# Optimization experiments

Measured on AMD Instinct MI355X. Metric: run time of the kernel, lower is better.

## Reference

```python
import jax, jax.numpy as jnp
import numpy as np

B, IN, C, M = 256, 512, 4, 6
S1, S2 = 255, 63          # neurons per layer excluding the prepended bias unit
K = 2 ** M                # contexts per neuron
P = 1e-3                  # pred_clipping
LMIN = float(np.log(P / (1.0 - P)))
LMAX = -LMIN
LR = 1e-3                 # constant learning rate
WCLIP = 5.0               # weight_clipping
BASE_BIAS = 0.0           # fixed base bias logit (original draws uniform in [LMIN, LMAX])


def setup_inputs() -> dict:
    key = jax.random.key(0)
    ks = jax.random.split(key, 10)
    x = jax.random.uniform(ks[0], (B, IN), dtype=jnp.float32)
    target = jax.random.randint(ks[1], (B,), 0, C, dtype=jnp.int32)
    cmaps1 = jax.random.normal(ks[2], (C, S1, M, IN), dtype=jnp.float32)
    w1 = jax.random.uniform(ks[3], (C, S1, K, IN), dtype=jnp.float32) * (2.0 / IN)
    bias1 = jax.random.uniform(ks[4], (1, 1, C), dtype=jnp.float32, minval=LMIN, maxval=LMAX)
    cmaps2 = jax.random.normal(ks[5], (C, S2, M, IN), dtype=jnp.float32)
    w2 = jax.random.uniform(ks[6], (C, S2, K, S1 + 1), dtype=jnp.float32) * (2.0 / (S1 + 1))
    bias2 = jax.random.uniform(ks[7], (1, 1, C), dtype=jnp.float32, minval=LMIN, maxval=LMAX)
    cmaps3 = jax.random.normal(ks[8], (C, 1, M, IN), dtype=jnp.float32)
    w3 = jax.random.uniform(ks[9], (C, 1, K, S2 + 1), dtype=jnp.float32) * (2.0 / (S2 + 1))
    return {"x": x, "target": target, "cmaps1": cmaps1, "w1": w1, "bias1": bias1,
            "cmaps2": cmaps2, "w2": w2, "bias2": bias2, "cmaps3": cmaps3, "w3": w3}


def _layer(logit3, context, tgt, cmaps, weights, bias):
    # logit3: (B, I, Cin) with Cin in {1, C}; context: (B, IN); tgt: (B, C) one-hot
    # cmaps: (C, S, M, IN); weights: (C, S, K, I)
    Cn, S = weights.shape[0], weights.shape[1]
    Bn = context.shape[0]
    # context halfspace gating -> per-(class, neuron, sample) context index
    dist = jnp.einsum('csmk,bk->csmb', cmaps, context)          # (C,S,M,B)
    conv = (2 ** jnp.arange(M, dtype=jnp.int32)).reshape(1, 1, M, 1)
    idx = jnp.sum((dist > 0.0).astype(jnp.int32) * conv, axis=2)  # (C,S,B)
    ci = jnp.arange(Cn)[:, None, None]
    si = jnp.arange(S)[None, :, None]
    sel = weights[ci, si, idx]                                  # gather: (C,S,B,I)
    lg = jnp.broadcast_to(logit3, (Bn, logit3.shape[1], Cn))    # (B,I,C)
    out = jnp.clip(jnp.einsum('csbi,bic->csb', sel, lg), LMIN, LMAX)
    out_t = jnp.transpose(out, (2, 1, 0))                       # (B,S,C)
    # online gradient-style update scattered back into the weight table
    diff = jax.nn.sigmoid(out_t) - tgt[:, None, :]              # (B,S,C)
    upd = LR * diff[..., None] * jnp.transpose(lg, (0, 2, 1))[:, None, :, :]  # (B,S,C,I)
    new_w = weights.at[ci, si, idx].set(
        jnp.clip(sel - jnp.transpose(upd, (2, 1, 0, 3)), -WCLIP, WCLIP))
    if bias is not None:
        out_t = jnp.concatenate([jnp.broadcast_to(bias, (Bn, 1, Cn)), out_t], axis=1)
    return out_t, new_w


def reference(x, target, cmaps1, w1, bias1, cmaps2, w2, bias2, cmaps3, w3):
    tgt = jax.nn.one_hot(target, C, dtype=x.dtype)              # (B,C)
    xb = jnp.clip(x, P, 1.0 - P)
    l0 = jnp.log(xb / (1.0 - xb)).at[:, 0].set(BASE_BIAS)       # base predictions in logit space
    out1, nw1 = _layer(l0[:, :, None], x, tgt, cmaps1, w1, bias1)  # (B,256,C)
    out2, nw2 = _layer(out1, x, tgt, cmaps2, w2, bias2)            # (B,64,C)
    out3, nw3 = _layer(out2, x, tgt, cmaps3, w3, None)             # (B,1,C)
    logits = out3[:, 0, :]                                         # (B,C)
    return (logits, nw1, nw2, nw3)
```

## Files before the change

### kernel.cpp

```cpp
#include <hip/hip_runtime.h>
#include <math.h>

#define B_   256
#define IN_  512
#define C_   4
#define M_   6
#define K_   64
#define S1_  255
#define S2_  63

#define NBLK1 (C_ * S1_)
#define NBLK2 (C_ * S2_)
#define NBLK3 (C_)
#define NBLK_ALL (NBLK1 + NBLK2 + NBLK3)

#define LMIN_ (-6.906754778648554f)
#define LMAX_ ( 6.906754778648554f)
#define LR_   0.001f
#define WCLIP_ 5.0f

typedef float v4f __attribute__((ext_vector_type(4)));

__device__ __forceinline__ float clampf(float v, float lo, float hi) {
    return fminf(fmaxf(v, lo), hi);
}

__global__ __launch_bounds__(256) void prep_kernel(const float* __restrict__ x,
                                                   const float* __restrict__ bias1,
                                                   const float* __restrict__ bias2,
                                                   float* __restrict__ xT,
                                                   float* __restrict__ l0,
                                                   float* __restrict__ l0T,
                                                   float* __restrict__ out1T,
                                                   float* __restrict__ out1RM,
                                                   float* __restrict__ out2T,
                                                   float* __restrict__ out2RM) {
    __shared__ float tx_[32][33];
    __shared__ float tl_[32][33];
    const int i0 = (blockIdx.x & 15) * 32;
    const int b0 = (blockIdx.x >> 4) * 32;
    const int tx = threadIdx.x & 31;
    const int ty = threadIdx.x >> 5;
#pragma unroll
    for (int r = 0; r < 4; ++r) {
        int bb = b0 + ty + 8 * r;
        int ii = i0 + tx;
        float xv = x[(size_t)bb * IN_ + ii];
        float xc = clampf(xv, 0.001f, 0.999f);
        float lv = (ii == 0) ? 0.0f : logf(xc / (1.0f - xc));
        l0[(size_t)bb * IN_ + ii] = lv;
        tx_[ty + 8 * r][tx] = xv;
        tl_[ty + 8 * r][tx] = lv;
    }
    __syncthreads();
#pragma unroll
    for (int r = 0; r < 4; ++r) {
        int ii = i0 + ty + 8 * r;
        int bb = b0 + tx;
        xT[(size_t)ii * B_ + bb]  = tx_[tx][ty + 8 * r];
        l0T[(size_t)ii * B_ + bb] = tl_[tx][ty + 8 * r];
    }
    int gid = blockIdx.x * 256 + threadIdx.x;
    if (gid < C_ * B_) {
        int c = gid >> 8, b = gid & 255;
        float b1 = bias1[c], b2 = bias2[c];
        out1T[((size_t)c * (S1_ + 1)) * B_ + b] = b1;
        out1RM[((size_t)c * B_ + b) * (S1_ + 1)] = b1;
        out2T[((size_t)c * (S2_ + 1)) * B_ + b] = b2;
        out2RM[((size_t)c * B_ + b) * (S2_ + 1)] = b2;
    }
}

__global__ __launch_bounds__(256) void route_kernel(
    const float* __restrict__ xT,
    const float* __restrict__ cmaps1,
    const float* __restrict__ cmaps2,
    const float* __restrict__ cmaps3,
    int* __restrict__ idx_buf)
{
    __shared__ float sacc[3][2][M_][B_];
    const int wv   = __builtin_amdgcn_readfirstlane(threadIdx.x >> 6);
    const int lane = threadIdx.x & 63;
    const int t0   = blockIdx.x * 2;

    const float* cmp[2];
#pragma unroll
    for (int u = 0; u < 2; ++u) {
        int bid = t0 + u;
        if (bid < NBLK1)              cmp[u] = cmaps1 + (size_t)bid * M_ * IN_;
        else if (bid < NBLK1 + NBLK2) cmp[u] = cmaps2 + (size_t)(bid - NBLK1) * M_ * IN_;
        else                          cmp[u] = cmaps3 + (size_t)(bid - NBLK1 - NBLK2) * M_ * IN_;
    }

    float acc[2][4][M_];
#pragma unroll
    for (int u = 0; u < 2; ++u)
#pragma unroll
        for (int jb = 0; jb < 4; ++jb)
#pragma unroll
            for (int m = 0; m < M_; ++m) acc[u][jb][m] = 0.0f;

    const int kw = wv * 128;
    for (int k0 = kw; k0 < kw + 128; k0 += 8) {
        float xv[8][4];
#pragma unroll
        for (int j = 0; j < 8; ++j)
#pragma unroll
            for (int jb = 0; jb < 4; ++jb)
                xv[j][jb] = xT[(size_t)(k0 + j) * B_ + 64 * jb + lane];
#pragma unroll
        for (int j = 0; j < 8; ++j)
#pragma unroll
            for (int u = 0; u < 2; ++u)
#pragma unroll
                for (int m = 0; m < M_; ++m) {
                    float cv = cmp[u][(size_t)m * IN_ + k0 + j];
#pragma unroll
                    for (int jb = 0; jb < 4; ++jb)
                        acc[u][jb][m] = fmaf(cv, xv[j][jb], acc[u][jb][m]);
                }
    }

    if (wv > 0) {
#pragma unroll
        for (int u = 0; u < 2; ++u)
#pragma unroll
            for (int jb = 0; jb < 4; ++jb)
#pragma unroll
                for (int m = 0; m < M_; ++m)
                    sacc[wv - 1][u][m][64 * jb + lane] = acc[u][jb][m];
    }
    __syncthreads();
    if (wv == 0) {
#pragma unroll
        for (int u = 0; u < 2; ++u)
#pragma unroll
            for (int jb = 0; jb < 4; ++jb) {
                int b = 64 * jb + lane;
                int myidx = 0;
#pragma unroll
                for (int m = 0; m < M_; ++m) {
                    float t = acc[u][jb][m] + sacc[0][u][m][b] + sacc[1][u][m][b] + sacc[2][u][m][b];
                    myidx |= (t > 0.0f) ? (1 << m) : 0;
                }
                idx_buf[(size_t)(t0 + u) * B_ + b] = myidx;
            }
    }
}

template<int DIN>
__device__ __forceinline__ void dotfin_body(
    int tile,
    const float* __restrict__ lgT, long lgT_sc,
    const float* __restrict__ w,
    const int* __restrict__ idx_buf,
    const int* __restrict__ target,
    float* __restrict__ onextT,
    float* __restrict__ onextRM,
    int* __restrict__ win_g,
    float* __restrict__ dw_g,
    int S,
    float* wl, float* part_s, float* diff_s, int* win_s)
{
    constexpr int HALF = DIN / 2;
    constexpr int NR   = HALF / 64;
    const int c   = tile / S;
    const int s   = tile - c * S;
    const int tid = threadIdx.x;
    const int kh  = __builtin_amdgcn_readfirstlane(tid >> 8);
    const int b   = tid & 255;

    if (tid < K_) win_s[tid] = -1;
    const int myrow = idx_buf[(size_t)tile * B_ + b];

    const float* wp  = w + (size_t)tile * K_ * DIN + kh * HALF;
    float*       dst = wl + kh * (K_ * 65);
    float dot = 0.0f;
#pragma unroll
    for (int r = 0; r < NR; ++r) {
        const float* src = wp + r * 64;
#pragma unroll
        for (int j = 0; j < 4; ++j) {
            int f   = b + 256 * j;
            int row = f >> 4;
            int q   = (f & 15) << 2;
            float4 v = *(const float4*)(src + (size_t)row * DIN + q);
            dst[row * 65 + q + 0] = v.x;
            dst[row * 65 + q + 1] = v.y;
            dst[row * 65 + q + 2] = v.z;
            dst[row * 65 + q + 3] = v.w;
        }
        __syncthreads();
        const float* lgp = lgT + (size_t)c * lgT_sc + (size_t)(kh * HALF + r * 64) * B_ + b;
        const float* wr  = dst + myrow * 65;
        for (int kk = 0; kk < 64; kk += 8) {
            float lv[8];
#pragma unroll
            for (int t = 0; t < 8; ++t) lv[t] = lgp[(size_t)(kk + t) * B_];
#pragma unroll
            for (int t = 0; t < 8; ++t) dot = fmaf(wr[kk + t], lv[t], dot);
        }
        __syncthreads();
    }
    if (kh == 1) part_s[b] = dot;
    __syncthreads();
    if (kh == 0) {
        float total = dot + part_s[b];
        float outv = clampf(total, LMIN_, LMAX_);
        onextT[((size_t)c * (S + 1) + (s + 1)) * B_ + b] = outv;
        onextRM[((size_t)c * B_ + b) * (size_t)(S + 1) + (s + 1)] = outv;
        float tg = (target[b] == c) ? 1.0f : 0.0f;
        diff_s[b] = 1.0f / (1.0f + expf(-outv)) - tg;
        atomicMax(&win_s[myrow], b);
    }
    __syncthreads();
    if (tid < K_) {
        int bw = win_s[tid];
        win_g[(size_t)tile * K_ + tid] = bw;
        dw_g[(size_t)tile * K_ + tid]  = (bw >= 0) ? LR_ * diff_s[bw] : 0.0f;
    }
}

template<int DIN>
__device__ __forceinline__ void update_body(
    int ub,
    const float* __restrict__ w,
    const float* __restrict__ lgRM, long lg_sc,
    const int* __restrict__ win_g,
    const float* __restrict__ dw_g,
    float* __restrict__ nw,
    int SK)
{
    constexpr int QPR = DIN / 4;
    constexpr int QSH = (DIN == 512) ? 7 : 6;
    const int base = ub * 2048 + threadIdx.x;
#pragma unroll
    for (int j = 0; j < 4; ++j) {
        int Q   = base + j * 512;
        int row = Q >> QSH;
        int col = (Q & (QPR - 1)) << 2;
        float4 wv = *(const float4*)(w + (size_t)row * DIN + col);
        int bw = win_g[row];
        if (bw >= 0) {
            float d = dw_g[row];
            int cc  = row / SK;
            const float4 lv = *(const float4*)(lgRM + (size_t)cc * lg_sc + (size_t)bw * DIN + col);
            wv.x = clampf(wv.x - d * lv.x, -WCLIP_, WCLIP_);
            wv.y = clampf(wv.y - d * lv.y, -WCLIP_, WCLIP_);
            wv.z = clampf(wv.z - d * lv.z, -WCLIP_, WCLIP_);
            wv.w = clampf(wv.w - d * lv.w, -WCLIP_, WCLIP_);
        }
        v4f o = {wv.x, wv.y, wv.z, wv.w};
        __builtin_nontemporal_store(o, (v4f*)(nw + (size_t)row * DIN + col));
    }
}

__global__ __launch_bounds__(512) void dotfin1_kernel(
    const float* __restrict__ l0T,
    const float* __restrict__ w1,
    const int* __restrict__ idx1,
    const int* __restrict__ target,
    float* __restrict__ out1T, float* __restrict__ out1RM,
    int* __restrict__ win1, float* __restrict__ dw1)
{
    __shared__ float wl[2 * K_ * 65];
    __shared__ float part_s[B_];
    __shared__ float diff_s[B_];
    __shared__ int   win_s[K_];
    dotfin_body<512>(blockIdx.x, l0T, 0L, w1, idx1, target,
                     out1T, out1RM, win1, dw1, S1_, wl, part_s, diff_s, win_s);
}

__global__ __launch_bounds__(512) void mix2_kernel(
    const float* __restrict__ out1T,
    const float* __restrict__ w2,
    const int* __restrict__ idx2,
    const int* __restrict__ target,
    float* __restrict__ out2T, float* __restrict__ out2RM,
    int* __restrict__ win2, float* __restrict__ dw2,
    const float* __restrict__ w1,
    const float* __restrict__ l0,
    const int* __restrict__ win1, const float* __restrict__ dw1,
    float* __restrict__ nw1, int ndot)
{
    __shared__ float wl[2 * K_ * 65];
    __shared__ float part_s[B_];
    __shared__ float diff_s[B_];
    __shared__ int   win_s[K_];
    if ((int)blockIdx.x < ndot)
        dotfin_body<256>(blockIdx.x, out1T, (long)(S1_ + 1) * B_, w2, idx2, target,
                         out2T, out2RM, win2, dw2, S2_, wl, part_s, diff_s, win_s);
    else
        update_body<512>(blockIdx.x - ndot, w1, l0, 0L, win1, dw1, nw1, S1_ * K_);
}

__device__ __forceinline__ void dotfinup3_body(
    int c,
    const float* __restrict__ lgT, long lgT_sc,
    const float* __restrict__ lgRM, long lg_sc,
    const float* __restrict__ w3,
    const int* __restrict__ idx3,
    const int* __restrict__ target,
    float* __restrict__ nw3,
    float* __restrict__ logits,
    float* wl , float* part_s, float* diff_s, float* dw_s, int* win_s)
{
    const int tid = threadIdx.x;
    const int kh  = __builtin_amdgcn_readfirstlane(tid >> 8);
    const int b   = tid & 255;
    if (tid < K_) win_s[tid] = -1;
    const int myrow = idx3[(size_t)c * B_ + b];

    const float* wp  = w3 + (size_t)c * K_ * 64 + kh * 32;
    float*       dst = wl + kh * (K_ * 33);
#pragma unroll
    for (int j = 0; j < 2; ++j) {
        int f   = b + 256 * j;
        int row = f >> 3;
        int q   = (f & 7) << 2;
        float4 v = *(const float4*)(wp + (size_t)row * 64 + q);
        dst[row * 33 + q + 0] = v.x;
        dst[row * 33 + q + 1] = v.y;
        dst[row * 33 + q + 2] = v.z;
        dst[row * 33 + q + 3] = v.w;
    }
    __syncthreads();
    const float* lgp = lgT + (size_t)c * lgT_sc + (size_t)(kh * 32) * B_ + b;
    const float* wr  = dst + myrow * 33;
    float dot = 0.0f;
    for (int kk = 0; kk < 32; kk += 8) {
        float lv[8];
#pragma unroll
        for (int t = 0; t < 8; ++t) lv[t] = lgp[(size_t)(kk + t) * B_];
#pragma unroll
        for (int t = 0; t < 8; ++t) dot = fmaf(wr[kk + t], lv[t], dot);
    }
    if (kh == 1) part_s[b] = dot;
    __syncthreads();
    if (kh == 0) {
        float total = dot + part_s[b];
        float outv = clampf(total, LMIN_, LMAX_);
        logits[(size_t)b * C_ + c] = outv;
        float tg = (target[b] == c) ? 1.0f : 0.0f;
        diff_s[b] = 1.0f / (1.0f + expf(-outv)) - tg;
        atomicMax(&win_s[myrow], b);
    }
    __syncthreads();
    if (tid < K_) dw_s[tid] = (win_s[tid] >= 0) ? LR_ * diff_s[win_s[tid]] : 0.0f;
    __syncthreads();

    const float* lgc = lgRM + (size_t)c * lg_sc;
    float* nwp = nw3 + (size_t)c * K_ * 64;
#pragma unroll
    for (int j = 0; j < 2; ++j) {
        int Q   = tid + 512 * j;
        int row = Q >> 4;
        int col = (Q & 15) << 2;
        const float* wsrc = wl + (col >> 5) * (K_ * 33) + row * 33 + (col & 31);
        float4 wv = {wsrc[0], wsrc[1], wsrc[2], wsrc[3]};
        int bw = win_s[row];
        if (bw >= 0) {
            float d = dw_s[row];
            const float4 lv = *(const float4*)(lgc + (size_t)bw * 64 + col);
            wv.x = clampf(wv.x - d * lv.x, -WCLIP_, WCLIP_);
            wv.y = clampf(wv.y - d * lv.y, -WCLIP_, WCLIP_);
            wv.z = clampf(wv.z - d * lv.z, -WCLIP_, WCLIP_);
            wv.w = clampf(wv.w - d * lv.w, -WCLIP_, WCLIP_);
        }
        v4f o = {wv.x, wv.y, wv.z, wv.w};
        __builtin_nontemporal_store(o, (v4f*)(nwp + (size_t)row * 64 + col));
    }
}

__global__ __launch_bounds__(512) void mix3_kernel(
    const float* __restrict__ out2T,
    const float* __restrict__ out2RM,
    const float* __restrict__ w3,
    const int* __restrict__ idx3,
    const int* __restrict__ target,
    float* __restrict__ nw3,
    float* __restrict__ logits,
    const float* __restrict__ w2,
    const float* __restrict__ out1RM,
    const int* __restrict__ win2, const float* __restrict__ dw2,
    float* __restrict__ nw2, int ndot)
{
    __shared__ float wl[2 * K_ * 33];
    __shared__ float part_s[B_];
    __shared__ float diff_s[B_];
    __shared__ float dw_s[K_];
    __shared__ int   win_s[K_];
    if ((int)blockIdx.x < ndot)
        dotfinup3_body(blockIdx.x, out2T, (long)(S2_ + 1) * B_,
                       out2RM, (long)B_ * (S2_ + 1), w3, idx3, target,
                       nw3, logits, wl, part_s, diff_s, dw_s, win_s);
    else
        update_body<256>(blockIdx.x - ndot, w2, out1RM, (long)B_ * (S1_ + 1),
                         win2, dw2, nw2, S2_ * K_);
}

extern "C" void kernel_launch(void* const* d_in, const int* in_sizes, int n_in,
                              void* d_out, int out_size, void* d_ws, size_t ws_size,
                              hipStream_t stream) {
    const float* x      = (const float*)d_in[0];
    const int*   target = (const int*)  d_in[1];
    const float* cmaps1 = (const float*)d_in[2];
    const float* w1     = (const float*)d_in[3];
    const float* bias1  = (const float*)d_in[4];
    const float* cmaps2 = (const float*)d_in[5];
    const float* w2     = (const float*)d_in[6];
    const float* bias2  = (const float*)d_in[7];
    const float* cmaps3 = (const float*)d_in[8];
    const float* w3     = (const float*)d_in[9];
    float* out = (float*)d_out;

    float* xT      = (float*)d_ws;
    float* l0      = xT     + (size_t)IN_ * B_;
    float* l0T     = l0     + (size_t)B_ * IN_;
    float* out1T   = l0T    + (size_t)IN_ * B_;
    float* out1RM  = out1T  + (size_t)C_ * (S1_ + 1) * B_;
    float* out2T   = out1RM + (size_t)C_ * B_ * (S1_ + 1);
    float* out2RM  = out2T  + (size_t)C_ * (S2_ + 1) * B_;
    float* dw_g    = out2RM + (size_t)C_ * B_ * (S2_ + 1);
    int*   win_g   = (int*)(dw_g + (size_t)NBLK_ALL * K_);
    int*   idx_buf = (int*)(win_g + (size_t)NBLK_ALL * K_);

    float* logits = out;
    float* nw1 = out + (size_t)B_ * C_;
    float* nw2 = nw1 + (size_t)C_ * S1_ * K_ * IN_;
    float* nw3 = nw2 + (size_t)C_ * S2_ * K_ * (S1_ + 1);

    const int* idx1 = idx_buf;
    const int* idx2 = idx_buf + (size_t)NBLK1 * B_;
    const int* idx3 = idx_buf + (size_t)(NBLK1 + NBLK2) * B_;
    int*   win1 = win_g;                float* dw1 = dw_g;
    int*   win2 = win_g + NBLK1 * K_;   float* dw2 = dw_g + NBLK1 * K_;

    prep_kernel<<<dim3(128), dim3(256), 0, stream>>>(
        x, bias1, bias2, xT, l0, l0T, out1T, out1RM, out2T, out2RM);

    route_kernel<<<dim3(NBLK_ALL / 2), dim3(256), 0, stream>>>(
        xT, cmaps1, cmaps2, cmaps3, idx_buf);

    dotfin1_kernel<<<dim3(NBLK1), dim3(512), 0, stream>>>(
        l0T, w1, idx1, target, out1T, out1RM, win1, dw1);

    mix2_kernel<<<dim3(NBLK2 + NBLK1 * 4), dim3(512), 0, stream>>>(
        out1T, w2, idx2, target, out2T, out2RM, win2, dw2,
        w1, l0, win1, dw1, nw1, NBLK2);

    mix3_kernel<<<dim3(NBLK3 + NBLK2 * 64 * 64 / 2048), dim3(512), 0, stream>>>(
        out2T, out2RM, w3, idx3, target, nw3, logits,
        w2, out1RM, win2, dw2, nw2, NBLK3);
}
```

Before: 126.6 us.

## Fuse layer-1 context routing into dot kernel and route layers 2-3 alongside

```diff
diff --git a/kernel.cpp b/kernel.cpp
--- a/kernel.cpp
+++ b/kernel.cpp
@@ -12,7 +12,7 @@
 #define NBLK1 (C_ * S1_)
 #define NBLK2 (C_ * S2_)
 #define NBLK3 (C_)
-#define NBLK_ALL (NBLK1 + NBLK2 + NBLK3)
+#define NBLK23 (NBLK2 + NBLK3)
 
 #define LMIN_ (-6.906754778648554f)
 #define LMAX_ ( 6.906754778648554f)
@@ -71,88 +71,13 @@
     }
 }
 
-__global__ __launch_bounds__(256) void route_kernel(
-    const float* __restrict__ xT,
-    const float* __restrict__ cmaps1,
-    const float* __restrict__ cmaps2,
-    const float* __restrict__ cmaps3,
-    int* __restrict__ idx_buf)
-{
-    __shared__ float sacc[3][2][M_][B_];
-    const int wv   = __builtin_amdgcn_readfirstlane(threadIdx.x >> 6);
-    const int lane = threadIdx.x & 63;
-    const int t0   = blockIdx.x * 2;
-
-    const float* cmp[2];
-#pragma unroll
-    for (int u = 0; u < 2; ++u) {
-        int bid = t0 + u;
-        if (bid < NBLK1)              cmp[u] = cmaps1 + (size_t)bid * M_ * IN_;
-        else if (bid < NBLK1 + NBLK2) cmp[u] = cmaps2 + (size_t)(bid - NBLK1) * M_ * IN_;
-        else                          cmp[u] = cmaps3 + (size_t)(bid - NBLK1 - NBLK2) * M_ * IN_;
-    }
-
-    float acc[2][4][M_];
-#pragma unroll
-    for (int u = 0; u < 2; ++u)
-#pragma unroll
-        for (int jb = 0; jb < 4; ++jb)
-#pragma unroll
-            for (int m = 0; m < M_; ++m) acc[u][jb][m] = 0.0f;
-
-    const int kw = wv * 128;
-    for (int k0 = kw; k0 < kw + 128; k0 += 8) {
-        float xv[8][4];
-#pragma unroll
-        for (int j = 0; j < 8; ++j)
-#pragma unroll
-            for (int jb = 0; jb < 4; ++jb)
-                xv[j][jb] = xT[(size_t)(k0 + j) * B_ + 64 * jb + lane];
-#pragma unroll
-        for (int j = 0; j < 8; ++j)
-#pragma unroll
-            for (int u = 0; u < 2; ++u)
-#pragma unroll
-                for (int m = 0; m < M_; ++m) {
-                    float cv = cmp[u][(size_t)m * IN_ + k0 + j];
-#pragma unroll
-                    for (int jb = 0; jb < 4; ++jb)
-                        acc[u][jb][m] = fmaf(cv, xv[j][jb], acc[u][jb][m]);
-                }
-    }
-
-    if (wv > 0) {
-#pragma unroll
-        for (int u = 0; u < 2; ++u)
-#pragma unroll
-            for (int jb = 0; jb < 4; ++jb)
-#pragma unroll
-                for (int m = 0; m < M_; ++m)
-                    sacc[wv - 1][u][m][64 * jb + lane] = acc[u][jb][m];
-    }
-    __syncthreads();
-    if (wv == 0) {
-#pragma unroll
-        for (int u = 0; u < 2; ++u)
-#pragma unroll
-            for (int jb = 0; jb < 4; ++jb) {
-                int b = 64 * jb + lane;
-                int myidx = 0;
-#pragma unroll
-                for (int m = 0; m < M_; ++m) {
-                    float t = acc[u][jb][m] + sacc[0][u][m][b] + sacc[1][u][m][b] + sacc[2][u][m][b];
-                    myidx |= (t > 0.0f) ? (1 << m) : 0;
-                }
-                idx_buf[(size_t)(t0 + u) * B_ + b] = myidx;
-            }
-    }
-}
-
-template<int DIN>
+template<int DIN, bool INLINE_ROUTE>
 __device__ __forceinline__ void dotfin_body(
     int tile,
     const float* __restrict__ lgT, long lgT_sc,
     const float* __restrict__ w,
+    const float* __restrict__ cmaps,
+    const float* __restrict__ xT,
     const int* __restrict__ idx_buf,
     const int* __restrict__ target,
     float* __restrict__ onextT,
@@ -160,7 +85,7 @@
     int* __restrict__ win_g,
     float* __restrict__ dw_g,
     int S,
-    float* wl, float* part_s, float* diff_s, int* win_s)
+    float* wl, float* part_s, float* diff_s, int* win_s, int* idx_s)
 {
     constexpr int HALF = DIN / 2;
     constexpr int NR   = HALF / 64;
@@ -171,7 +96,43 @@
     const int b   = tid & 255;
 
     if (tid < K_) win_s[tid] = -1;
-    const int myrow = idx_buf[(size_t)tile * B_ + b];
+
+    int myrow;
+    if (INLINE_ROUTE) {
+        const float* cmp = cmaps + (size_t)tile * M_ * IN_;
+        float racc[M_];
+#pragma unroll
+        for (int m = 0; m < M_; ++m) racc[m] = 0.0f;
+        const int kw = kh * 256;
+        for (int k0 = kw; k0 < kw + 256; k0 += 8) {
+            float xv[8];
+#pragma unroll
+            for (int j = 0; j < 8; ++j) xv[j] = xT[(size_t)(k0 + j) * B_ + b];
+#pragma unroll
+            for (int j = 0; j < 8; ++j)
+#pragma unroll
+                for (int m = 0; m < M_; ++m)
+                    racc[m] = fmaf(cmp[(size_t)m * IN_ + kw + (k0 - kw) + j], xv[j], racc[m]);
+        }
+        if (kh == 1) {
+#pragma unroll
+            for (int m = 0; m < M_; ++m) wl[m * B_ + b] = racc[m];
+        }
+        __syncthreads();
+        if (kh == 0) {
+            int myidx = 0;
+#pragma unroll
+            for (int m = 0; m < M_; ++m) {
+                float t = racc[m] + wl[m * B_ + b];
+                myidx |= (t > 0.0f) ? (1 << m) : 0;
+            }
+            idx_s[b] = myidx;
+        }
+        __syncthreads();
+        myrow = idx_s[b];
+    } else {
+        myrow = idx_buf[(size_t)tile * B_ + b];
+    }
 
     const float* wp  = w + (size_t)tile * K_ * DIN + kh * HALF;
     float*       dst = wl + kh * (K_ * 65);
@@ -219,6 +180,95 @@
         win_g[(size_t)tile * K_ + tid] = bw;
         dw_g[(size_t)tile * K_ + tid]  = (bw >= 0) ? LR_ * diff_s[bw] : 0.0f;
     }
+}
+
+__device__ __forceinline__ void route23_body(
+    int rb,
+    const float* __restrict__ xT,
+    const float* __restrict__ cmaps2,
+    const float* __restrict__ cmaps3,
+    int* __restrict__ idx23,
+    float* wl)
+{
+    const int tid = threadIdx.x;
+    const float* cmp = (rb < NBLK2) ? cmaps2 + (size_t)rb * M_ * IN_
+                                    : cmaps3 + (size_t)(rb - NBLK2) * M_ * IN_;
+    float acc[4][M_];
+    int wv = 0, lane = 0;
+    if (tid < 256) {
+        wv   = __builtin_amdgcn_readfirstlane(tid >> 6);
+        lane = tid & 63;
+#pragma unroll
+        for (int jb = 0; jb < 4; ++jb)
+#pragma unroll
+            for (int m = 0; m < M_; ++m) acc[jb][m] = 0.0f;
+        const int kw = wv * 128;
+        for (int k0 = kw; k0 < kw + 128; k0 += 8) {
+            float xv[8][4];
+#pragma unroll
+            for (int j = 0; j < 8; ++j)
+#pragma unroll
+                for (int jb = 0; jb < 4; ++jb)
+                    xv[j][jb] = xT[(size_t)(k0 + j) * B_ + 64 * jb + lane];
+#pragma unroll
+            for (int j = 0; j < 8; ++j)
+#pragma unroll
+                for (int m = 0; m < M_; ++m) {
+                    float cv = cmp[(size_t)m * IN_ + k0 + j];
+#pragma unroll
+                    for (int jb = 0; jb < 4; ++jb)
+                        acc[jb][m] = fmaf(cv, xv[j][jb], acc[jb][m]);
+                }
+        }
+        if (wv > 0) {
+#pragma unroll
+            for (int jb = 0; jb < 4; ++jb)
+#pragma unroll
+                for (int m = 0; m < M_; ++m)
+                    wl[((wv - 1) * M_ + m) * B_ + 64 * jb + lane] = acc[jb][m];
+        }
+    }
+    __syncthreads();
+    if (tid < 256 && wv == 0) {
+#pragma unroll
+        for (int jb = 0; jb < 4; ++jb) {
+            int b = 64 * jb + lane;
+            int myidx = 0;
+#pragma unroll
+            for (int m = 0; m < M_; ++m) {
+                float t = acc[jb][m] + wl[(0 * M_ + m) * B_ + b]
+                                     + wl[(1 * M_ + m) * B_ + b]
+                                     + wl[(2 * M_ + m) * B_ + b];
+                myidx |= (t > 0.0f) ? (1 << m) : 0;
+            }
+            idx23[(size_t)rb * B_ + b] = myidx;
+        }
+    }
+}
+
+__global__ __launch_bounds__(512) void fusedL1_kernel(
+    const float* __restrict__ xT,
+    const float* __restrict__ l0T,
+    const float* __restrict__ cmaps1,
+    const float* __restrict__ cmaps2,
+    const float* __restrict__ cmaps3,
+    const float* __restrict__ w1,
+    const int* __restrict__ target,
+    float* __restrict__ out1T, float* __restrict__ out1RM,
+    int* __restrict__ win1, float* __restrict__ dw1,
+    int* __restrict__ idx23)
+{
+    __shared__ float wl[2 * K_ * 65];
+    __shared__ float part_s[B_];
+    __shared__ float diff_s[B_];
+    __shared__ int   win_s[K_];
+    __shared__ int   idx_s[B_];
+    if ((int)blockIdx.x < NBLK1)
+        dotfin_body<512, true>(blockIdx.x, l0T, 0L, w1, cmaps1, xT, nullptr, target,
+                               out1T, out1RM, win1, dw1, S1_,
+                               wl, part_s, diff_s, win_s, idx_s);
+    else
+        route23_body(blockIdx.x - NBLK1, xT, cmaps2, cmaps3, idx23, wl);
 }
 
 template<int DIN>
@@ -255,22 +305,6 @@
     }
 }
 
-__global__ __launch_bounds__(512) void dotfin1_kernel(
-    const float* __restrict__ l0T,
-    const float* __restrict__ w1,
-    const int* __restrict__ idx1,
-    const int* __restrict__ target,
-    float* __restrict__ out1T, float* __restrict__ out1RM,
-    int* __restrict__ win1, float* __restrict__ dw1)
-{
-    __shared__ float wl[2 * K_ * 65];
-    __shared__ float part_s[B_];
-    __shared__ float diff_s[B_];
-    __shared__ int   win_s[K_];
-    dotfin_body<512>(blockIdx.x, l0T, 0L, w1, idx1, target,
-                     out1T, out1RM, win1, dw1, S1_, wl, part_s, diff_s, win_s);
-}
-
 __global__ __launch_bounds__(512) void mix2_kernel(
     const float* __restrict__ out1T,
     const float* __restrict__ w2,
@@ -281,17 +315,20 @@
     const float* __restrict__ w1,
     const float* __restrict__ l0,
     const int* __restrict__ win1, const float* __restrict__ dw1,
-    float* __restrict__ nw1, int ndot)
+    float* __restrict__ nw1)
 {
     __shared__ float wl[2 * K_ * 65];
     __shared__ float part_s[B_];
     __shared__ float diff_s[B_];
     __shared__ int   win_s[K_];
-    if ((int)blockIdx.x < ndot)
-        dotfin_body<256>(blockIdx.x, out1T, (long)(S1_ + 1) * B_, w2, idx2, target,
-                         out2T, out2RM, win2, dw2, S2_, wl, part_s, diff_s, win_s);
+    __shared__ int   idx_s[B_];
+    if ((int)blockIdx.x < NBLK2)
+        dotfin_body<256, false>(blockIdx.x, out1T, (long)(S1_ + 1) * B_, w2,
+                                nullptr, nullptr, idx2, target,
+                                out2T, out2RM, win2, dw2, S2_,
+                                wl, part_s, diff_s, win_s, idx_s);
     else
-        update_body<512>(blockIdx.x - ndot, w1, l0, 0L, win1, dw1, nw1, S1_ * K_);
+        update_body<512>(blockIdx.x - NBLK2, w1, l0, 0L, win1, dw1, nw1, S1_ * K_);
 }
 
 __device__ __forceinline__ void dotfinup3_body(
@@ -383,19 +420,19 @@
     const float* __restrict__ w2,
     const float* __restrict__ out1RM,
     const int* __restrict__ win2, const float* __restrict__ dw2,
-    float* __restrict__ nw2, int ndot)
+    float* __restrict__ nw2)
 {
     __shared__ float wl[2 * K_ * 33];
     __shared__ float part_s[B_];
     __shared__ float diff_s[B_];
     __shared__ float dw_s[K_];
     __shared__ int   win_s[K_];
-    if ((int)blockIdx.x < ndot)
+    if ((int)blockIdx.x < NBLK3)
         dotfinup3_body(blockIdx.x, out2T, (long)(S2_ + 1) * B_,
                        out2RM, (long)B_ * (S2_ + 1), w3, idx3, target,
                        nw3, logits, wl, part_s, diff_s, dw_s, win_s);
     else
-        update_body<256>(blockIdx.x - ndot, w2, out1RM, (long)B_ * (S1_ + 1),
+        update_body<256>(blockIdx.x - NBLK3, w2, out1RM, (long)B_ * (S1_ + 1),
                          win2, dw2, nw2, S2_ * K_);
 }
 
@@ -422,34 +459,31 @@
     float* out2T   = out1RM + (size_t)C_ * B_ * (S1_ + 1);
     float* out2RM  = out2T  + (size_t)C_ * (S2_ + 1) * B_;
     float* dw_g    = out2RM + (size_t)C_ * B_ * (S2_ + 1);
-    int*   win_g   = (int*)(dw_g + (size_t)NBLK_ALL * K_);
-    int*   idx_buf = (int*)(win_g + (size_t)NBLK_ALL * K_);
+    int*   win_g   = (int*)(dw_g + (size_t)(NBLK1 + NBLK2) * K_);
+    int*   idx23   = (int*)(win_g + (size_t)(NBLK1 + NBLK2) * K_);
 
     float* logits = out;
     float* nw1 = out + (size_t)B_ * C_;
     float* nw2 = nw1 + (size_t)C_ * S1_ * K_ * IN_;
     float* nw3 = nw2 + (size_t)C_ * S2_ * K_ * (S1_ + 1);
 
-    const int* idx1 = idx_buf;
-    const int* idx2 = idx_buf + (size_t)NBLK1 * B_;
-    const int* idx3 = idx_buf + (size_t)(NBLK1 + NBLK2) * B_;
     int*   win1 = win_g;                float* dw1 = dw_g;
     int*   win2 = win_g + NBLK1 * K_;   float* dw2 = dw_g + NBLK1 * K_;
+    const int* idx2 = idx23;
+    const int* idx3 = idx23 + (size_t)NBLK2 * B_;
 
     prep_kernel<<<dim3(128), dim3(256), 0, stream>>>(
         x, bias1, bias2, xT, l0, l0T, out1T, out1RM, out2T, out2RM);
 
-    route_kernel<<<dim3(NBLK_ALL / 2), dim3(256), 0, stream>>>(
-        xT, cmaps1, cmaps2, cmaps3, idx_buf);
-
-    dotfin1_kernel<<<dim3(NBLK1), dim3(512), 0, stream>>>(
-        l0T, w1, idx1, target, out1T, out1RM, win1, dw1);
+    fusedL1_kernel<<<dim3(NBLK1 + NBLK23), dim3(512), 0, stream>>>(
+        xT, l0T, cmaps1, cmaps2, cmaps3, w1, target,
+        out1T, out1RM, win1, dw1, idx23);
 
     mix2_kernel<<<dim3(NBLK2 + NBLK1 * 4), dim3(512), 0, stream>>>(
         out1T, w2, idx2, target, out2T, out2RM, win2, dw2,
-        w1, l0, win1, dw1, nw1, NBLK2);
-
-    mix3_kernel<<<dim3(NBLK3 + NBLK2 * 64 * 64 / 2048), dim3(512), 0, stream>>>(
+        w1, l0, win1, dw1, nw1);
+
+    mix3_kernel<<<dim3(NBLK3 + NBLK2 * 2), dim3(512), 0, stream>>>(
         out2T, out2RM, w3, idx3, target, nw3, logits,
-        w2, out1RM, win2, dw2, nw2, NBLK3);
-}
+        w2, out1RM, win2, dw2, nw2);
+}
```

New measurement: 139.8 us. 1.1x slower.

## Fuse per-tile weight update into layer dot kernels, drop global win/dw buffers

Applied to the files above, without the earlier changes.

```diff
diff --git a/kernel.cpp b/kernel.cpp
--- a/kernel.cpp
+++ b/kernel.cpp
@@ -149,21 +149,23 @@
 }
 
 template<int DIN>
-__device__ __forceinline__ void dotfin_body(
+__device__ __forceinline__ void layerfused_body(
     int tile,
     const float* __restrict__ lgT, long lgT_sc,
+    const float* __restrict__ lgRM, long lg_sc,
     const float* __restrict__ w,
+    float* __restrict__ nw,
     const int* __restrict__ idx_buf,
     const int* __restrict__ target,
     float* __restrict__ onextT,
     float* __restrict__ onextRM,
-    int* __restrict__ win_g,
-    float* __restrict__ dw_g,
     int S,
-    float* wl, float* part_s, float* diff_s, int* win_s)
+    float* wl, float* part_s, float* diff_s, float* dw_s, int* win_s)
 {
     constexpr int HALF = DIN / 2;
     constexpr int NR   = HALF / 64;
+    constexpr int QPR  = DIN / 4;
+    constexpr int QSH  = (DIN == 512) ? 7 : 6;
     const int c   = tile / S;
     const int s   = tile - c * S;
     const int tid = threadIdx.x;
@@ -202,6 +204,7 @@
         }
         __syncthreads();
     }
+
     if (kh == 1) part_s[b] = dot;
     __syncthreads();
     if (kh == 0) {
@@ -214,97 +217,69 @@
         atomicMax(&win_s[myrow], b);
     }
     __syncthreads();
-    if (tid < K_) {
-        int bw = win_s[tid];
-        win_g[(size_t)tile * K_ + tid] = bw;
-        dw_g[(size_t)tile * K_ + tid]  = (bw >= 0) ? LR_ * diff_s[bw] : 0.0f;
-    }
-}
-
-template<int DIN>
-__device__ __forceinline__ void update_body(
-    int ub,
-    const float* __restrict__ w,
-    const float* __restrict__ lgRM, long lg_sc,
-    const int* __restrict__ win_g,
-    const float* __restrict__ dw_g,
-    float* __restrict__ nw,
-    int SK)
-{
-    constexpr int QPR = DIN / 4;
-    constexpr int QSH = (DIN == 512) ? 7 : 6;
-    const int base = ub * 2048 + threadIdx.x;
-#pragma unroll
-    for (int j = 0; j < 4; ++j) {
-        int Q   = base + j * 512;
+    if (tid < K_) dw_s[tid] = (win_s[tid] >= 0) ? LR_ * diff_s[win_s[tid]] : 0.0f;
+    __syncthreads();
+
+    const float* lgc = lgRM + (size_t)c * lg_sc;
+    const float* wp0 = w  + (size_t)tile * K_ * DIN;
+    float*       nwp = nw + (size_t)tile * K_ * DIN;
+#pragma unroll
+    for (int j = 0; j < (K_ * QPR) / 512; ++j) {
+        int Q   = tid + 512 * j;
         int row = Q >> QSH;
         int col = (Q & (QPR - 1)) << 2;
-        float4 wv = *(const float4*)(w + (size_t)row * DIN + col);
-        int bw = win_g[row];
+        float4 wv = *(const float4*)(wp0 + (size_t)row * DIN + col);
+        int bw = win_s[row];
         if (bw >= 0) {
-            float d = dw_g[row];
-            int cc  = row / SK;
-            const float4 lv = *(const float4*)(lgRM + (size_t)cc * lg_sc + (size_t)bw * DIN + col);
+            float d = dw_s[row];
+            const float4 lv = *(const float4*)(lgc + (size_t)bw * DIN + col);
             wv.x = clampf(wv.x - d * lv.x, -WCLIP_, WCLIP_);
             wv.y = clampf(wv.y - d * lv.y, -WCLIP_, WCLIP_);
             wv.z = clampf(wv.z - d * lv.z, -WCLIP_, WCLIP_);
             wv.w = clampf(wv.w - d * lv.w, -WCLIP_, WCLIP_);
         }
         v4f o = {wv.x, wv.y, wv.z, wv.w};
-        __builtin_nontemporal_store(o, (v4f*)(nw + (size_t)row * DIN + col));
-    }
-}
-
-__global__ __launch_bounds__(512) void dotfin1_kernel(
-    const float* __restrict__ l0T,
-    const float* __restrict__ w1,
-    const int* __restrict__ idx1,
+        __builtin_nontemporal_store(o, (v4f*)(nwp + (size_t)row * DIN + col));
+    }
+}
+
+template<int DIN>
+__global__ __launch_bounds__(512) void layerfused_kernel(
+    const float* __restrict__ lgT, long lgT_sc,
+    const float* __restrict__ lgRM, long lg_sc,
+    const float* __restrict__ w,
+    float* __restrict__ nw,
+    const int* __restrict__ idx_buf,
     const int* __restrict__ target,
-    float* __restrict__ out1T, float* __restrict__ out1RM,
-    int* __restrict__ win1, float* __restrict__ dw1)
+    float* __restrict__ onextT,
+    float* __restrict__ onextRM,
+    int S)
 {
     __shared__ float wl[2 * K_ * 65];
     __shared__ float part_s[B_];
     __shared__ float diff_s[B_];
+    __shared__ float dw_s[K_];
     __shared__ int   win_s[K_];
-    dotfin_body<512>(blockIdx.x, l0T, 0L, w1, idx1, target,
-                     out1T, out1RM, win1, dw1, S1_, wl, part_s, diff_s, win_s);
-}
-
-__global__ __launch_bounds__(512) void mix2_kernel(
-    const float* __restrict__ out1T,
-    const float* __restrict__ w2,
-    const int* __restrict__ idx2,
-    const int* __restrict__ target,
-    float* __restrict__ out2T, float* __restrict__ out2RM,
-    int* __restrict__ win2, float* __restrict__ dw2,
-    const float* __restrict__ w1,
-    const float* __restrict__ l0,
-    const int* __restrict__ win1, const float* __restrict__ dw1,
-    float* __restrict__ nw1, int ndot)
-{
-    __shared__ float wl[2 * K_ * 65];
-    __shared__ float part_s[B_];
-    __shared__ float diff_s[B_];
-    __shared__ int   win_s[K_];
-    if ((int)blockIdx.x < ndot)
-        dotfin_body<256>(blockIdx.x, out1T, (long)(S1_ + 1) * B_, w2, idx2, target,
-                         out2T, out2RM, win2, dw2, S2_, wl, part_s, diff_s, win_s);
-    else
-        update_body<512>(blockIdx.x - ndot, w1, l0, 0L, win1, dw1, nw1, S1_ * K_);
-}
-
-__device__ __forceinline__ void dotfinup3_body(
-    int c,
-    const float* __restrict__ lgT, long lgT_sc,
-    const float* __restrict__ lgRM, long lg_sc,
+    layerfused_body<DIN>(blockIdx.x, lgT, lgT_sc, lgRM, lg_sc, w, nw,
+                         idx_buf, target, onextT, onextRM, S,
+                         wl, part_s, diff_s, dw_s, win_s);
+}
+
+__global__ __launch_bounds__(512) void layer3_kernel(
+    const float* __restrict__ out2T,
+    const float* __restrict__ out2RM,
     const float* __restrict__ w3,
     const int* __restrict__ idx3,
     const int* __restrict__ target,
     float* __restrict__ nw3,
-    float* __restrict__ logits,
-    float* wl , float* part_s, float* diff_s, float* dw_s, int* win_s)
+    float* __restrict__ logits)
 {
+    __shared__ float wl[2 * K_ * 33];
+    __shared__ float part_s[B_];
+    __shared__ float diff_s[B_];
+    __shared__ float dw_s[K_];
+    __shared__ int   win_s[K_];
+    const int c   = blockIdx.x;
     const int tid = threadIdx.x;
     const int kh  = __builtin_amdgcn_readfirstlane(tid >> 8);
     const int b   = tid & 255;
@@ -325,7 +300,7 @@
         dst[row * 33 + q + 3] = v.w;
     }
     __syncthreads();
-    const float* lgp = lgT + (size_t)c * lgT_sc + (size_t)(kh * 32) * B_ + b;
+    const float* lgp = out2T + (size_t)c * (S2_ + 1) * B_ + (size_t)(kh * 32) * B_ + b;
     const float* wr  = dst + myrow * 33;
     float dot = 0.0f;
     for (int kk = 0; kk < 32; kk += 8) {
@@ -349,7 +324,7 @@
     if (tid < K_) dw_s[tid] = (win_s[tid] >= 0) ? LR_ * diff_s[win_s[tid]] : 0.0f;
     __syncthreads();
 
-    const float* lgc = lgRM + (size_t)c * lg_sc;
+    const float* lgc = out2RM + (size_t)c * B_ * (S2_ + 1);
     float* nwp = nw3 + (size_t)c * K_ * 64;
 #pragma unroll
     for (int j = 0; j < 2; ++j) {
@@ -372,33 +347,6 @@
     }
 }
 
-__global__ __launch_bounds__(512) void mix3_kernel(
-    const float* __restrict__ out2T,
-    const float* __restrict__ out2RM,
-    const float* __restrict__ w3,
-    const int* __restrict__ idx3,
-    const int* __restrict__ target,
-    float* __restrict__ nw3,
-    float* __restrict__ logits,
-    const float* __restrict__ w2,
-    const float* __restrict__ out1RM,
-    const int* __restrict__ win2, const float* __restrict__ dw2,
-    float* __restrict__ nw2, int ndot)
-{
-    __shared__ float wl[2 * K_ * 33];
-    __shared__ float part_s[B_];
-    __shared__ float diff_s[B_];
-    __shared__ float dw_s[K_];
-    __shared__ int   win_s[K_];
-    if ((int)blockIdx.x < ndot)
-        dotfinup3_body(blockIdx.x, out2T, (long)(S2_ + 1) * B_,
-                       out2RM, (long)B_ * (S2_ + 1), w3, idx3, target,
-                       nw3, logits, wl, part_s, diff_s, dw_s, win_s);
-    else
-        update_body<256>(blockIdx.x - ndot, w2, out1RM, (long)B_ * (S1_ + 1),
-                         win2, dw2, nw2, S2_ * K_);
-}
-
 extern "C" void kernel_launch(void* const* d_in, const int* in_sizes, int n_in,
                               void* d_out, int out_size, void* d_ws, size_t ws_size,
                               hipStream_t stream) {
@@ -421,9 +369,7 @@
     float* out1RM  = out1T  + (size_t)C_ * (S1_ + 1) * B_;
     float* out2T   = out1RM + (size_t)C_ * B_ * (S1_ + 1);
     float* out2RM  = out2T  + (size_t)C_ * (S2_ + 1) * B_;
-    float* dw_g    = out2RM + (size_t)C_ * B_ * (S2_ + 1);
-    int*   win_g   = (int*)(dw_g + (size_t)NBLK_ALL * K_);
-    int*   idx_buf = (int*)(win_g + (size_t)NBLK_ALL * K_);
+    int*   idx_buf = (int*)(out2RM + (size_t)C_ * B_ * (S2_ + 1));
 
     float* logits = out;
     float* nw1 = out + (size_t)B_ * C_;
@@ -433,8 +379,6 @@
     const int* idx1 = idx_buf;
     const int* idx2 = idx_buf + (size_t)NBLK1 * B_;
     const int* idx3 = idx_buf + (size_t)(NBLK1 + NBLK2) * B_;
-    int*   win1 = win_g;                float* dw1 = dw_g;
-    int*   win2 = win_g + NBLK1 * K_;   float* dw2 = dw_g + NBLK1 * K_;
 
     prep_kernel<<<dim3(128), dim3(256), 0, stream>>>(
         x, bias1, bias2, xT, l0, l0T, out1T, out1RM, out2T, out2RM);
@@ -442,14 +386,13 @@
     route_kernel<<<dim3(NBLK_ALL / 2), dim3(256), 0, stream>>>(
         xT, cmaps1, cmaps2, cmaps3, idx_buf);
 
-    dotfin1_kernel<<<dim3(NBLK1), dim3(512), 0, stream>>>(
-        l0T, w1, idx1, target, out1T, out1RM, win1, dw1);
-
-    mix2_kernel<<<dim3(NBLK2 + NBLK1 * 4), dim3(512), 0, stream>>>(
-        out1T, w2, idx2, target, out2T, out2RM, win2, dw2,
-        w1, l0, win1, dw1, nw1, NBLK2);
-
-    mix3_kernel<<<dim3(NBLK3 + NBLK2 * 64 * 64 / 2048), dim3(512), 0, stream>>>(
-        out2T, out2RM, w3, idx3, target, nw3, logits,
-        w2, out1RM, win2, dw2, nw2, NBLK3);
-}
+    layerfused_kernel<512><<<dim3(NBLK1), dim3(512), 0, stream>>>(
+        l0T, 0L, l0, 0L, w1, nw1, idx1, target, out1T, out1RM, S1_);
+
+    layerfused_kernel<256><<<dim3(NBLK2), dim3(512), 0, stream>>>(
+        out1T, (long)(S1_ + 1) * B_, out1RM, (long)B_ * (S1_ + 1),
+        w2, nw2, idx2, target, out2T, out2RM, S2_);
+
+    layer3_kernel<<<dim3(NBLK3), dim3(512), 0, stream>>>(
+        out2T, out2RM, w3, idx3, target, nw3, logits);
+}
```

Result: slower. 131.4 us (+3.8%).
